# Performance work log

Hardware: AMD Instinct MI355X
Metric: run time of the kernel (lower is better)

The kernel has to match this reference:

```python
import jax, jax.numpy as jnp
import numpy as np
from jax import lax

EPS = 1e-5
DW_THRESH = 4.0
PW_THRESH = 0.001
C_IN = 512
C_OUT = 512


def setup_inputs() -> dict:
    key = jax.random.key(0)
    ks = jax.random.split(key, 8)
    B, H, W = 64, 28, 28
    x = jax.random.normal(ks[0], (B, C_IN, H, W), dtype=jnp.float32)
    # depthwise 3x3 kernel, OIHW with feature_group_count=C_IN -> (C_IN, 1, 3, 3)
    dw_w = jax.random.normal(ks[1], (C_IN, 1, 3, 3), dtype=jnp.float32) * 0.1
    dw_b = jax.random.normal(ks[2], (C_IN,), dtype=jnp.float32) * 0.1
    bn1_g = jnp.ones((C_IN,), jnp.float32)
    bn1_b = jnp.zeros((C_IN,), jnp.float32)
    bn1_m = jnp.zeros((C_IN,), jnp.float32)
    bn1_v = jnp.ones((C_IN,), jnp.float32)
    # pointwise 1x1 kernel
    pw_w = jax.random.normal(ks[3], (C_OUT, C_IN, 1, 1), dtype=jnp.float32) * 0.05
    pw_b = jax.random.normal(ks[4], (C_OUT,), dtype=jnp.float32) * 0.1
    bn2_g = jnp.ones((C_OUT,), jnp.float32)
    bn2_b = jnp.zeros((C_OUT,), jnp.float32)
    bn2_m = jnp.zeros((C_OUT,), jnp.float32)
    bn2_v = jnp.ones((C_OUT,), jnp.float32)
    return dict(x=x, dw_w=dw_w, dw_b=dw_b, bn1_g=bn1_g, bn1_b=bn1_b,
                bn1_m=bn1_m, bn1_v=bn1_v, pw_w=pw_w, pw_b=pw_b,
                bn2_g=bn2_g, bn2_b=bn2_b, bn2_m=bn2_m, bn2_v=bn2_v)


def _bn(x, g, b, m, v):
    # inference batchnorm over channel axis 1 of NCHW
    inv = g * lax.rsqrt(v + EPS)
    return x * inv[None, :, None, None] + (b - m * inv)[None, :, None, None]


def _prune(x, thresh):
    # per-(batch, channel) magnitude pruning: zero the whole HxW plane if
    # max(|x[b,c]|) < thresh  (matches torch max(max, -min))
    amax = jnp.max(jnp.abs(x), axis=(2, 3), keepdims=True)
    return jnp.where(amax < thresh, jnp.zeros_like(x), x)


def reference(x, dw_w, dw_b, bn1_g, bn1_b, bn1_m, bn1_v,
              pw_w, pw_b, bn2_g, bn2_b, bn2_m, bn2_v):
    dn = ('NCHW', 'OIHW', 'NCHW')
    # depthwise conv, stride 1, padding 1, groups = C_IN
    h = lax.conv_general_dilated(x, dw_w, window_strides=(1, 1),
                                 padding=((1, 1), (1, 1)),
                                 feature_group_count=C_IN,
                                 dimension_numbers=dn)
    h = h + dw_b[None, :, None, None]
    h = jax.nn.relu(_bn(h, bn1_g, bn1_b, bn1_m, bn1_v))
    h = _prune(h, DW_THRESH)
    # pointwise 1x1 conv
    h = lax.conv_general_dilated(h, pw_w, window_strides=(1, 1),
                                 padding=((0, 0), (0, 0)),
                                 dimension_numbers=dn)
    h = h + pw_b[None, :, None, None]
    h = jax.nn.relu(_bn(h, bn2_g, bn2_b, bn2_m, bn2_v))
    h = _prune(h, PW_THRESH)
    return h
```

## Files before the change

### kernel.cpp

```cpp
#include <hip/hip_runtime.h>

#define EPS        1e-5f
#define DW_THRESH  4.0f
#define PW_THRESH  0.001f
#define CIN        512
#define COUT       512
#define HWPLANE    784

typedef float floatx4 __attribute__((ext_vector_type(4)));

__global__ __launch_bounds__(256) void dw_flags_kernel(
    const float* __restrict__ x,
    const float* __restrict__ dw_w, const float* __restrict__ dw_b,
    const float* __restrict__ bn1_g, const float* __restrict__ bn1_b,
    const float* __restrict__ bn1_m, const float* __restrict__ bn1_v,
    unsigned int* __restrict__ mask)
{
    const int bid  = blockIdx.x;
    const int word = bid & 15;
    const int tid  = threadIdx.x;
    const int wv   = tid >> 6;
    const int lane = tid & 63;

    __shared__ float tile[4][30 * 28];
    __shared__ float2 sAB[32];
    __shared__ unsigned int wflags[4];

    float* tp = tile[wv] + 28;

    if (tid < 32) {
        const int   c    = word * 32 + tid;
        const float inv1 = bn1_g[c] * rsqrtf(bn1_v[c] + EPS);
        const float c1   = (dw_b[c] - bn1_m[c]) * inv1 + bn1_b[c];
        float S = 0.0f;
        #pragma unroll
        for (int k = 0; k < 9; ++k) S += fabsf(dw_w[c * 9 + k]);
        sAB[tid] = make_float2(fabsf(inv1) * S, c1);
    }
    if (lane < 28)      tile[wv][lane] = 0.0f;
    else if (lane < 56) tile[wv][29 * 28 + lane - 28] = 0.0f;
    __syncthreads();

    const float* xw = x + ((size_t)bid * 32 + (size_t)wv * 8) * HWPLANE;

    const int   j   = lane % 14;
    const int   gg  = lane / 14;
    const int   r0  = (gg < 4 ? gg : 3) * 7;
    const float mLm = (j > 0)  ? 1.0f : 0.0f;
    const float mRm = (j < 13) ? 1.0f : 0.0f;
    const int   pL  = (j > 0)  ? 2 * j - 2 : 0;
    const int   pC  = 2 * j;
    const int   pR  = (j < 13) ? 2 * j + 2 : 24;

    float4 v0 = ((const float4*)xw)[lane];
    float4 v1 = ((const float4*)xw)[lane + 64];
    float4 v2 = ((const float4*)xw)[lane + 128];
    float4 v3 = ((const float4*)xw)[192 + (lane & 3)];

    unsigned int flags = 0;

    for (int p = 0; p < 8; ++p) {
        float4 n0, n1, n2, n3;
        if (p < 7) {
            const float* xn = xw + (size_t)(p + 1) * HWPLANE;
            n0 = ((const float4*)xn)[lane];
            n1 = ((const float4*)xn)[lane + 64];
            n2 = ((const float4*)xn)[lane + 128];
            n3 = ((const float4*)xn)[192 + (lane & 3)];
        }

        float m = fmaxf(fmaxf(fmaxf(fabsf(v0.x), fabsf(v0.y)),
                              fmaxf(fabsf(v0.z), fabsf(v0.w))),
                        fmaxf(fmaxf(fabsf(v1.x), fabsf(v1.y)),
                              fmaxf(fabsf(v1.z), fabsf(v1.w))));
        m = fmaxf(m, fmaxf(fmaxf(fabsf(v2.x), fabsf(v2.y)),
                           fmaxf(fabsf(v2.z), fabsf(v2.w))));
        m = fmaxf(m, fmaxf(fmaxf(fabsf(v3.x), fabsf(v3.y)),
                           fmaxf(fabsf(v3.z), fabsf(v3.w))));

        const float2 ab  = sAB[wv * 8 + p];
        const bool   hot = fmaf(ab.x, m, ab.y) >= DW_THRESH * 0.999f;

        if (__any(hot)) {
            const int   c    = word * 32 + wv * 8 + p;
            const float inv1 = bn1_g[c] * rsqrtf(bn1_v[c] + EPS);
            const float c1   = (dw_b[c] - bn1_m[c]) * inv1 + bn1_b[c];
            float w9[9];
            #pragma unroll
            for (int k = 0; k < 9; ++k) w9[k] = dw_w[c * 9 + k];

            ((float4*)tp)[lane]       = v0;
            ((float4*)tp)[lane + 64]  = v1;
            ((float4*)tp)[lane + 128] = v2;
            if (lane < 4) ((float4*)tp)[lane + 192] = v3;

            float amax_l = 0.0f;
            float2 La = *(const float2*)&tp[(r0 - 1) * 28 + pL];
            float2 Ca = *(const float2*)&tp[(r0 - 1) * 28 + pC];
            float2 Ra = *(const float2*)&tp[(r0 - 1) * 28 + pR];
            float2 Lb = *(const float2*)&tp[r0 * 28 + pL];
            float2 Cb = *(const float2*)&tp[r0 * 28 + pC];
            float2 Rb = *(const float2*)&tp[r0 * 28 + pR];
            float am1 = La.y * mLm, a0 = Ca.x, a1 = Ca.y, a2 = Ra.x * mRm;
            float bm1 = Lb.y * mLm, b0 = Cb.x, b1 = Cb.y, b2 = Rb.x * mRm;
            #pragma unroll
            for (int rr = 0; rr < 7; ++rr) {
                const int rc = r0 + rr + 1;
                float2 Lc = *(const float2*)&tp[rc * 28 + pL];
                float2 Cc = *(const float2*)&tp[rc * 28 + pC];
                float2 Rc = *(const float2*)&tp[rc * 28 + pR];
                float cm1 = Lc.y * mLm, cc0 = Cc.x, cc1 = Cc.y, cc2 = Rc.x * mRm;
                float acc0 =              w9[0] * am1;
                acc0 = fmaf(w9[1], a0,  acc0);
                acc0 = fmaf(w9[2], a1,  acc0);
                acc0 = fmaf(w9[3], bm1, acc0);
                acc0 = fmaf(w9[4], b0,  acc0);
                acc0 = fmaf(w9[5], b1,  acc0);
                acc0 = fmaf(w9[6], cm1, acc0);
                acc0 = fmaf(w9[7], cc0, acc0);
                acc0 = fmaf(w9[8], cc1, acc0);
                float acc1 =              w9[0] * a0;
                acc1 = fmaf(w9[1], a1,  acc1);
                acc1 = fmaf(w9[2], a2,  acc1);
                acc1 = fmaf(w9[3], b0,  acc1);
                acc1 = fmaf(w9[4], b1,  acc1);
                acc1 = fmaf(w9[5], b2,  acc1);
                acc1 = fmaf(w9[6], cc0, acc1);
                acc1 = fmaf(w9[7], cc1, acc1);
                acc1 = fmaf(w9[8], cc2, acc1);
                const float t0 = fmaf(acc0, inv1, c1);
                const float t1 = fmaf(acc1, inv1, c1);
                amax_l = fmaxf(amax_l, fmaxf(t0, t1));
                am1 = bm1; a0 = b0; a1 = b1; a2 = b2;
                bm1 = cm1; b0 = cc0; b1 = cc1; b2 = cc2;
            }
            #pragma unroll
            for (int off = 1; off < 64; off <<= 1)
                amax_l = fmaxf(amax_l, __shfl_xor(amax_l, off, 64));
            if (amax_l >= DW_THRESH) flags |= (1u << p);
        }

        if (p < 7) { v0 = n0; v1 = n1; v2 = n2; v3 = n3; }
    }

    if (lane == 0) wflags[wv] = flags;
    __syncthreads();
    if (tid == 0)
        mask[bid] = wflags[0] | (wflags[1] << 8) | (wflags[2] << 16)
                  | (wflags[3] << 24);
}

__global__ __launch_bounds__(256) void pw_kernel(
    const float* __restrict__ x,
    const float* __restrict__ dw_w, const float* __restrict__ dw_b,
    const float* __restrict__ bn1_g, const float* __restrict__ bn1_b,
    const float* __restrict__ bn1_m, const float* __restrict__ bn1_v,
    const float* __restrict__ pw_w, const float* __restrict__ pw_b,
    const float* __restrict__ bn2_g, const float* __restrict__ bn2_b,
    const float* __restrict__ bn2_m, const float* __restrict__ bn2_v,
    const unsigned int* __restrict__ mask,
    float* __restrict__ out)
{
    const int bid = blockIdx.x;
    const int b   = bid >> 4;
    const int og  = bid & 15;
    const int tid = threadIdx.x;

    __shared__ unsigned int smask[16];
    __shared__ float sconst[32];
    __shared__ float sx[30 * 30];
    __shared__ float red[4];
    __shared__ float sfinal;

    if (tid < 16) smask[tid] = mask[(b << 4) + tid];
    __syncthreads();

    unsigned int any = 0;
    #pragma unroll
    for (int k = 0; k < 16; ++k) any |= smask[k];

    float* ob = out + (size_t)bid * 32 * HWPLANE;

    if (any == 0u) {
        if (tid < 32) {
            const int   co   = og * 32 + tid;
            const float inv2 = bn2_g[co] * rsqrtf(bn2_v[co] + EPS);
            const float c2   = (pw_b[co] - bn2_m[co]) * inv2 + bn2_b[co];
            float vv = c2 > 0.0f ? c2 : 0.0f;
            if (vv < PW_THRESH) vv = 0.0f;
            sconst[tid] = vv;
        }
        __syncthreads();
        floatx4* obv = (floatx4*)ob;
        for (int jj = tid; jj < 6272; jj += 256) {
            const float vv = sconst[jj / 196];
            floatx4 t = {vv, vv, vv, vv};
            __builtin_nontemporal_store(t, &obv[jj]);
        }
        return;
    }

    for (int i = tid; i < 900; i += 256) sx[i] = 0.0f;
    const int xx = tid % 28;
    const int ys = (tid / 28) * 4;

    for (int col = 0; col < 32; ++col) {
        const int co = og * 32 + col;
        const float inv2 = bn2_g[co] * rsqrtf(bn2_v[co] + EPS);
        const float c2   = (pw_b[co] - bn2_m[co]) * inv2 + bn2_b[co];
        float acc[4] = {0.f, 0.f, 0.f, 0.f};

        for (int ci = 0; ci < CIN; ++ci) {
            if (!((smask[ci >> 5] >> (ci & 31)) & 1u)) continue;
            __syncthreads();
            const float* xp = x + ((size_t)(b * CIN + ci)) * HWPLANE;
            if (tid < 196) {
                const float4 vv = ((const float4*)xp)[tid];
                const int y  = tid / 7;
                const int x0 = (tid % 7) * 4;
                float* d = &sx[(y + 1) * 30 + x0 + 1];
                d[0] = vv.x; d[1] = vv.y; d[2] = vv.z; d[3] = vv.w;
            }
            const float inv1 = bn1_g[ci] * rsqrtf(bn1_v[ci] + EPS);
            const float c1   = (dw_b[ci] - bn1_m[ci]) * inv1 + bn1_b[ci];
            const float wco  = pw_w[co * CIN + ci];
            float w9[9];
            #pragma unroll
            for (int k = 0; k < 9; ++k) w9[k] = dw_w[ci * 9 + k];
            __syncthreads();
            if (tid < 196) {
                float r[6][3];
                #pragma unroll
                for (int jj = 0; jj < 6; ++jj)
                    #pragma unroll
                    for (int k = 0; k < 3; ++k)
                        r[jj][k] = sx[(ys + jj) * 30 + xx + k];
                #pragma unroll
                for (int i = 0; i < 4; ++i) {
                    float a = 0.0f;
                    #pragma unroll
                    for (int dy = 0; dy < 3; ++dy)
                        #pragma unroll
                        for (int dx = 0; dx < 3; ++dx)
                            a = fmaf(w9[dy * 3 + dx], r[i + dy][dx], a);
                    float hv = fmaf(a, inv1, c1);
                    hv = hv > 0.0f ? hv : 0.0f;
                    acc[i] = fmaf(wco, hv, acc[i]);
                }
            }
        }

        float vout[4];
        float amax = 0.0f;
        if (tid < 196) {
            #pragma unroll
            for (int i = 0; i < 4; ++i) {
                float t = fmaf(acc[i], inv2, c2);
                t = t > 0.0f ? t : 0.0f;
                vout[i] = t;
                amax = fmaxf(amax, t);
            }
        }
        #pragma unroll
        for (int off = 32; off > 0; off >>= 1)
            amax = fmaxf(amax, __shfl_down(amax, off, 64));
        if ((tid & 63) == 0) red[tid >> 6] = amax;
        __syncthreads();
        if (tid == 0)
            sfinal = fmaxf(fmaxf(red[0], red[1]), fmaxf(red[2], red[3]));
        __syncthreads();
        const bool zero = sfinal < PW_THRESH;
        if (tid < 196) {
            float* op = ob + (size_t)col * HWPLANE;
            #pragma unroll
            for (int i = 0; i < 4; ++i)
                op[(ys + i) * 28 + xx] = zero ? 0.0f : vout[i];
        }
        __syncthreads();
    }
}

extern "C" void kernel_launch(void* const* d_in, const int* in_sizes, int n_in,
                              void* d_out, int out_size, void* d_ws, size_t ws_size,
                              hipStream_t stream)
{
    const float* x     = (const float*)d_in[0];
    const float* dw_w  = (const float*)d_in[1];
    const float* dw_b  = (const float*)d_in[2];
    const float* bn1_g = (const float*)d_in[3];
    const float* bn1_b = (const float*)d_in[4];
    const float* bn1_m = (const float*)d_in[5];
    const float* bn1_v = (const float*)d_in[6];
    const float* pw_w  = (const float*)d_in[7];
    const float* pw_b  = (const float*)d_in[8];
    const float* bn2_g = (const float*)d_in[9];
    const float* bn2_b = (const float*)d_in[10];
    const float* bn2_m = (const float*)d_in[11];
    const float* bn2_v = (const float*)d_in[12];

    unsigned int* mask = (unsigned int*)d_ws;

    dw_flags_kernel<<<64 * 16, 256, 0, stream>>>(
        x, dw_w, dw_b, bn1_g, bn1_b, bn1_m, bn1_v, mask);

    pw_kernel<<<64 * 16, 256, 0, stream>>>(
        x, dw_w, dw_b, bn1_g, bn1_b, bn1_m, bn1_v,
        pw_w, pw_b, bn2_g, bn2_b, bn2_m, bn2_v,
        mask, (float*)d_out);
}
```

Before: 41.80 us.

## Fuse constant output fill into flag kernel and make second kernel fixup-only

The first kernel now computes the per-output-channel constant (bias, BN2, ReLU, prune) and writes the constant planes for its block while it also computes the depthwise prune flags. The second kernel becomes a fixup that returns at once when a batch has no surviving channels, and only does the pointwise path otherwise. The goal is to overlap the large output write with the input read in one pass, instead of running the write as a separate phase after the flag kernel. The fill now uses plain float4 stores rather than nontemporal stores. When any flag is set, the output is written twice.

```diff
diff --git a/kernel.cpp b/kernel.cpp
--- a/kernel.cpp
+++ b/kernel.cpp
@@ -7,14 +7,16 @@
 #define COUT       512
 #define HWPLANE    784
 
-typedef float floatx4 __attribute__((ext_vector_type(4)));
-
-__global__ __launch_bounds__(256) void dw_flags_kernel(
+__global__ __launch_bounds__(256) void flags_fill_kernel(
     const float* __restrict__ x,
     const float* __restrict__ dw_w, const float* __restrict__ dw_b,
     const float* __restrict__ bn1_g, const float* __restrict__ bn1_b,
     const float* __restrict__ bn1_m, const float* __restrict__ bn1_v,
-    unsigned int* __restrict__ mask)
+    const float* __restrict__ pw_b,
+    const float* __restrict__ bn2_g, const float* __restrict__ bn2_b,
+    const float* __restrict__ bn2_m, const float* __restrict__ bn2_v,
+    unsigned int* __restrict__ mask,
+    float* __restrict__ out)
 {
     const int bid  = blockIdx.x;
     const int word = bid & 15;
@@ -24,6 +26,7 @@
 
     __shared__ float tile[4][30 * 28];
     __shared__ float2 sAB[32];
+    __shared__ float  sconst[32];
     __shared__ unsigned int wflags[4];
 
     float* tp = tile[wv] + 28;
@@ -36,6 +39,12 @@
         #pragma unroll
         for (int k = 0; k < 9; ++k) S += fabsf(dw_w[c * 9 + k]);
         sAB[tid] = make_float2(fabsf(inv1) * S, c1);
+
+        const float inv2 = bn2_g[c] * rsqrtf(bn2_v[c] + EPS);
+        const float c2   = (pw_b[c] - bn2_m[c]) * inv2 + bn2_b[c];
+        float vv = c2 > 0.0f ? c2 : 0.0f;
+        if (vv < PW_THRESH) vv = 0.0f;
+        sconst[tid] = vv;
     }
     if (lane < 28)      tile[wv][lane] = 0.0f;
     else if (lane < 56) tile[wv][29 * 28 + lane - 28] = 0.0f;
@@ -148,9 +157,15 @@
     if (tid == 0)
         mask[bid] = wflags[0] | (wflags[1] << 8) | (wflags[2] << 16)
                   | (wflags[3] << 24);
+
+    float* ob = out + (size_t)bid * 32 * HWPLANE;
+    for (int jj = tid; jj < 6272; jj += 256) {
+        const float vv = sconst[jj / 196];
+        ((float4*)ob)[jj] = make_float4(vv, vv, vv, vv);
+    }
 }
 
-__global__ __launch_bounds__(256) void pw_kernel(
+__global__ __launch_bounds__(256) void fixup_kernel(
     const float* __restrict__ x,
     const float* __restrict__ dw_w, const float* __restrict__ dw_b,
     const float* __restrict__ bn1_g, const float* __restrict__ bn1_b,
@@ -167,7 +182,6 @@
     const int tid = threadIdx.x;
 
     __shared__ unsigned int smask[16];
-    __shared__ float sconst[32];
     __shared__ float sx[30 * 30];
     __shared__ float red[4];
     __shared__ float sfinal;
@@ -178,29 +192,12 @@
     unsigned int any = 0;
     #pragma unroll
     for (int k = 0; k < 16; ++k) any |= smask[k];
+    if (any == 0u) return;
 
     float* ob = out + (size_t)bid * 32 * HWPLANE;
 
-    if (any == 0u) {
-        if (tid < 32) {
-            const int   co   = og * 32 + tid;
-            const float inv2 = bn2_g[co] * rsqrtf(bn2_v[co] + EPS);
-            const float c2   = (pw_b[co] - bn2_m[co]) * inv2 + bn2_b[co];
-            float vv = c2 > 0.0f ? c2 : 0.0f;
-            if (vv < PW_THRESH) vv = 0.0f;
-            sconst[tid] = vv;
-        }
-        __syncthreads();
-        floatx4* obv = (floatx4*)ob;
-        for (int jj = tid; jj < 6272; jj += 256) {
-            const float vv = sconst[jj / 196];
-            floatx4 t = {vv, vv, vv, vv};
-            __builtin_nontemporal_store(t, &obv[jj]);
-        }
-        return;
-    }
-
     for (int i = tid; i < 900; i += 256) sx[i] = 0.0f;
+    __syncthreads();
     const int xx = tid % 28;
     const int ys = (tid / 28) * 4;
 
@@ -299,12 +296,13 @@
     const float* bn2_v = (const float*)d_in[12];
 
     unsigned int* mask = (unsigned int*)d_ws;
-
-    dw_flags_kernel<<<64 * 16, 256, 0, stream>>>(
-        x, dw_w, dw_b, bn1_g, bn1_b, bn1_m, bn1_v, mask);
-
-    pw_kernel<<<64 * 16, 256, 0, stream>>>(
+    float* out = (float*)d_out;
+
+    flags_fill_kernel<<<64 * 16, 256, 0, stream>>>(
         x, dw_w, dw_b, bn1_g, bn1_b, bn1_m, bn1_v,
-        pw_w, pw_b, bn2_g, bn2_b, bn2_m, bn2_v,
-        mask, (float*)d_out);
+        pw_b, bn2_g, bn2_b, bn2_m, bn2_v, mask, out);
+
+    fixup_kernel<<<64 * 16, 256, 0, stream>>>(
+        x, dw_w, dw_b, bn1_g, bn1_b, bn1_m, bn1_v,
+        pw_w, pw_b, bn2_g, bn2_b, bn2_m, bn2_v, mask, out);
 }
```

After: 34.95 us. 1.2x faster.
